# Optimization experiments

Measured on AMD Instinct MI355X. Metric: run time of the kernel, lower is better.

The kernel has to match this reference:

```python
import jax, jax.numpy as jnp
import numpy as np

KS = 63      # Gaussian kernel size (module default)
SIGMA = 32.0 # Gaussian sigma (module default)


def _gaussian_kernel2d(k, sigma):
    # kornia get_gaussian_kernel2d: outer product of normalized 1D gaussians
    x = jnp.arange(k, dtype=jnp.float32) - k // 2
    g = jnp.exp(-(x * x) / (2.0 * sigma * sigma))
    g = g / g.sum()
    return jnp.outer(g, g)  # [k,k]


def _filter2d_constant(x, k2d):
    # kornia filter2d, border_type='constant' (zero pad), depthwise per channel
    C = x.shape[1]
    kern = jnp.broadcast_to(k2d, (C, 1) + k2d.shape)  # [C,1,k,k]
    return jax.lax.conv_general_dilated(
        x, kern, window_strides=(1, 1), padding='SAME',
        dimension_numbers=('NCHW', 'OIHW', 'NCHW'), feature_group_count=C)


def _grid_sample_bilinear(img, grid, align_corners=False):
    # torch.nn.functional.grid_sample, mode='bilinear', padding_mode='zeros'
    B, C, H, W = img.shape
    gx, gy = grid[..., 0], grid[..., 1]
    if align_corners:
        x = (gx + 1.0) * (W - 1) * 0.5
        y = (gy + 1.0) * (H - 1) * 0.5
    else:
        x = ((gx + 1.0) * W - 1.0) * 0.5
        y = ((gy + 1.0) * H - 1.0) * 0.5
    x0 = jnp.floor(x); y0 = jnp.floor(y)
    x0i = x0.astype(jnp.int32); y0i = y0.astype(jnp.int32)
    x1i = x0i + 1; y1i = y0i + 1
    wx1 = x - x0; wx0 = 1.0 - wx1
    wy1 = y - y0; wy0 = 1.0 - wy1

    def gather(iy, ix):
        valid = ((ix >= 0) & (ix < W) & (iy >= 0) & (iy < H))
        iyc = jnp.clip(iy, 0, H - 1)
        ixc = jnp.clip(ix, 0, W - 1)
        # per-batch fancy gather: [B,C,H,W]
        v = jax.vmap(lambda im, yy, xx: im[:, yy, xx])(img, iyc, ixc)
        return v * valid[:, None].astype(img.dtype)

    out = (gather(y0i, x0i) * (wy0 * wx0)[:, None]
           + gather(y0i, x1i) * (wy0 * wx1)[:, None]
           + gather(y1i, x0i) * (wy1 * wx0)[:, None]
           + gather(y1i, x1i) * (wy1 * wx1)[:, None])
    return out


def setup_inputs() -> dict:
    key = jax.random.key(0)
    k1, k2 = jax.random.split(key)
    image = jax.random.normal(k1, (8, 3, 512, 512), dtype=jnp.float32)
    noise = jax.random.uniform(k2, (8, 2, 512, 512), dtype=jnp.float32)
    return {"image": image, "noise": noise}


def reference(image, noise):
    B, C, H, W = image.shape
    noise = noise * 2.0 - 1.0                      # rand*2-1 as in forward()
    k2d = _gaussian_kernel2d(KS, SIGMA)
    disp_xy = _filter2d_constant(noise, k2d)       # [B,2,H,W]
    disp = jnp.transpose(disp_xy, (0, 2, 3, 1))    # [B,H,W,2] (x,y)
    # kornia create_meshgrid(normalized_coordinates=True): linspace(-1,1)
    xs = jnp.linspace(-1.0, 1.0, W, dtype=image.dtype)
    ys = jnp.linspace(-1.0, 1.0, H, dtype=image.dtype)
    base = jnp.stack(jnp.meshgrid(xs, ys, indexing='xy'), axis=-1)  # [H,W,2]
    grid = jnp.clip(base[None] + disp, -1.0, 1.0)
    warped = _grid_sample_bilinear(image, grid, align_corners=False)
    return warped, disp
```

## Files before the change

### kernel.cpp

```cpp
#include <hip/hip_runtime.h>
#include <math.h>

#define KS 63
#define RAD 31
#define NB 8
#define NC 3
#define NH 512
#define NW 512
#define PADH 576
#define TILE_H 32
#define TILE_W 32
#define ROWS 94

struct GaussW { float w[KS]; };

__global__ __launch_bounds__(256) void hblur_kernel(const float* __restrict__ noise,
                                                    float* __restrict__ tmp, GaussW gw) {
    const int bid = blockIdx.x;
    const int t = threadIdx.x;
    if (bid >= NB * NH) {
        const int pid = bid - NB * NH;
        const int img = pid >> 5;
        const int pr  = pid & 31;
        const int row = (pr < 16) ? (pr * 2) : (544 + (pr - 16) * 2);
        float4* dst = (float4*)(tmp + ((size_t)img * PADH + row) * NW);
        dst[t] = make_float4(0.f, 0.f, 0.f, 0.f);
        return;
    }
    const int b = bid >> 9;
    const int h = bid & (NH - 1);
    const int ch = t >> 7;
    const int tt = t & 127;

    __shared__ float rows[2][PADH];
    const float* src = noise + ((size_t)(b * 2 + ch) * NH + h) * NW;
    {
        const float4 nv = *(const float4*)(src + 4 * tt);
        float4 sv;
        sv.x = fmaf(nv.x, 2.f, -1.f); sv.y = fmaf(nv.y, 2.f, -1.f);
        sv.z = fmaf(nv.z, 2.f, -1.f); sv.w = fmaf(nv.w, 2.f, -1.f);
        *(float4*)&rows[ch][32 + 4 * tt] = sv;
        if (tt < 8) {
            *(float4*)&rows[ch][4 * tt]       = make_float4(0.f, 0.f, 0.f, 0.f);
            *(float4*)&rows[ch][544 + 4 * tt] = make_float4(0.f, 0.f, 0.f, 0.f);
        }
    }
    __syncthreads();

    float acc[4] = {0.f, 0.f, 0.f, 0.f};
#pragma unroll
    for (int c = 0; c < 17; ++c) {
        const float4 v = *(const float4*)&rows[ch][4 * tt + 4 * c];
        const float vv[4] = {v.x, v.y, v.z, v.w};
#pragma unroll
        for (int e = 0; e < 4; ++e) {
#pragma unroll
            for (int oo = 0; oo < 4; ++oo) {
                const int j = 4 * c + e - oo - 1;
                if (j >= 0 && j < KS) acc[oo] = fmaf(vv[e], gw.w[j], acc[oo]);
            }
        }
    }
    float4* dst = (float4*)(tmp + (((size_t)(b * 2 + ch) * PADH) + 32 + h) * NW + 4 * tt);
    *dst = make_float4(acc[0], acc[1], acc[2], acc[3]);
}

__global__ __launch_bounds__(256) void vwarp_kernel(const float* __restrict__ tmp,
                                                    const float* __restrict__ img,
                                                    float2* __restrict__ disp,
                                                    float* __restrict__ warped,
                                                    GaussW gw) {
    const int t = threadIdx.x;
    int bid = blockIdx.x;
    bid = (bid & 7) * 256 + (bid >> 3);
    const int b   = bid >> 8;
    const int rem = bid & 255;
    const int ht  = rem >> 4;
    const int wt  = rem & 15;
    const int H0 = ht * TILE_H;
    const int W0 = wt * TILE_W;

    __shared__ float lds[2][ROWS][TILE_W];

    const float* g0 = tmp + ((size_t)(b * 2) * PADH + H0 + 1) * NW + W0;
    const size_t choff = (size_t)PADH * NW;
    for (int idx = t; idx < 2 * ROWS * (TILE_W / 4); idx += 256) {
        const int c4   = idx & 7;
        const int rowc = idx >> 3;
        const int c = (rowc >= ROWS) ? 1 : 0;
        const int r = rowc - ROWS * c;
        const float4 v = *(const float4*)(g0 + (size_t)c * choff + (size_t)r * NW + c4 * 4);
        *(float4*)&lds[c][r][c4 * 4] = v;
    }
    __syncthreads();

    const int w  = t & 31;
    const int lh = (t >> 5) * 4;

    float ax[4] = {0.f, 0.f, 0.f, 0.f};
    float ay[4] = {0.f, 0.f, 0.f, 0.f};
#pragma unroll
    for (int rr = 0; rr < 66; ++rr) {
        const float vx = lds[0][lh + rr][w];
        const float vy = lds[1][lh + rr][w];
#pragma unroll
        for (int o = 0; o < 4; ++o) {
            const int j = rr - o;
            if (j >= 0 && j < KS) {
                ax[o] = fmaf(vx, gw.w[j], ax[o]);
                ay[o] = fmaf(vy, gw.w[j], ay[o]);
            }
        }
    }

    const int wg = W0 + w;
    const float gxb = fmaf((float)wg, 2.0f / 511.0f, -1.0f);
    const float* i0 = img + (size_t)b * NC * NH * NW;
    const float* i1 = i0 + NH * NW;
    const float* i2 = i1 + NH * NW;
    float* wp = warped + (size_t)b * NC * NH * NW;

#pragma unroll
    for (int o = 0; o < 4; ++o) {
        const int h = H0 + lh + o;
        disp[((size_t)b * NH + h) * NW + wg] = make_float2(ax[o], ay[o]);

        float gx = gxb + ax[o];
        float gy = fmaf((float)h, 2.0f / 511.0f, -1.0f) + ay[o];
        gx = fminf(1.f, fmaxf(-1.f, gx));
        gy = fminf(1.f, fmaxf(-1.f, gy));

        const float x = ((gx + 1.0f) * (float)NW - 1.0f) * 0.5f;
        const float y = ((gy + 1.0f) * (float)NH - 1.0f) * 0.5f;
        const float xf = floorf(x), yf = floorf(y);
        const int x0 = (int)xf, y0 = (int)yf;
        const int x1 = x0 + 1,  y1 = y0 + 1;
        const float wx1 = x - xf, wx0 = 1.0f - wx1;
        const float wy1 = y - yf, wy0 = 1.0f - wy1;
        const float fx0 = ((unsigned)x0 < NW) ? 1.f : 0.f;
        const float fx1 = ((unsigned)x1 < NW) ? 1.f : 0.f;
        const float fy0 = ((unsigned)y0 < NH) ? 1.f : 0.f;
        const float fy1 = ((unsigned)y1 < NH) ? 1.f : 0.f;
        const int x0c = min(max(x0, 0), NW - 1), x1c = min(max(x1, 0), NW - 1);
        const int y0c = min(max(y0, 0), NH - 1), y1c = min(max(y1, 0), NH - 1);
        const float w00 = wy0 * wx0 * (fy0 * fx0), w01 = wy0 * wx1 * (fy0 * fx1);
        const float w10 = wy1 * wx0 * (fy1 * fx0), w11 = wy1 * wx1 * (fy1 * fx1);
        const int o00 = y0c * NW + x0c, o01 = y0c * NW + x1c;
        const int o10 = y1c * NW + x0c, o11 = y1c * NW + x1c;
        const size_t po = (size_t)h * NW + wg;
        wp[po]               = ((i0[o00] * w00 + i0[o01] * w01) + i0[o10] * w10) + i0[o11] * w11;
        wp[NH * NW + po]     = ((i1[o00] * w00 + i1[o01] * w01) + i1[o10] * w10) + i1[o11] * w11;
        wp[2 * NH * NW + po] = ((i2[o00] * w00 + i2[o01] * w01) + i2[o10] * w10) + i2[o11] * w11;
    }
}

extern "C" void kernel_launch(void* const* d_in, const int* in_sizes, int n_in,
                              void* d_out, int out_size, void* d_ws, size_t ws_size,
                              hipStream_t stream) {
    const float* image = (const float*)d_in[0];
    const float* noise = (const float*)d_in[1];
    float* warped = (float*)d_out;
    float* dispo  = (float*)d_out + (size_t)NB * NC * NH * NW;
    float* scratch = (float*)d_ws;

    GaussW gw;
    float s = 0.f;
    for (int i = 0; i < KS; ++i) {
        const float xv = (float)(i - RAD);
        gw.w[i] = expf(-(xv * xv) / (2.0f * 32.0f * 32.0f));
        s += gw.w[i];
    }
    for (int i = 0; i < KS; ++i) gw.w[i] /= s;

    hblur_kernel<<<NB * NH + 512, 256, 0, stream>>>(noise, scratch, gw);
    vwarp_kernel<<<NB * (NH / TILE_H) * (NW / TILE_W), 256, 0, stream>>>(
        scratch, image, (float2*)dispo, warped, gw);
}
```

Measured before the change: 136.5 us.

## Widen vertical-warp tiles to 64 columns with 4-wide vectorized per-thread work

The vertical blur and warp kernel now uses 32x64 tiles. Each thread computes 2 rows by 4 adjacent columns, reading float4 values from LDS and writing disp and warped outputs with float4 stores. This cuts LDS reads and store instructions per output and shares each LDS value across fewer redundant loads. The horizontal blur kernel also interleaves batches in its block-to-row mapping. In exchange, LDS use per block doubles and fewer blocks are launched, which can lower occupancy, and the 4-pixel gathers per thread are more serialized.

```diff
diff --git a/kernel.cpp b/kernel.cpp
--- a/kernel.cpp
+++ b/kernel.cpp
@@ -9,7 +9,7 @@
 #define NW 512
 #define PADH 576
 #define TILE_H 32
-#define TILE_W 32
+#define TILE_W 64
 #define ROWS 94
 
 struct GaussW { float w[KS]; };
@@ -27,8 +27,8 @@
         dst[t] = make_float4(0.f, 0.f, 0.f, 0.f);
         return;
     }
-    const int b = bid >> 9;
-    const int h = bid & (NH - 1);
+    const int b = bid & 7;
+    const int h = (bid >> 3) & (NH - 1);
     const int ch = t >> 7;
     const int tt = t & 127;
 
@@ -72,11 +72,11 @@
                                                     GaussW gw) {
     const int t = threadIdx.x;
     int bid = blockIdx.x;
-    bid = (bid & 7) * 256 + (bid >> 3);
-    const int b   = bid >> 8;
-    const int rem = bid & 255;
-    const int ht  = rem >> 4;
-    const int wt  = rem & 15;
+    bid = (bid & 7) * 128 + (bid >> 3);
+    const int b   = bid >> 7;
+    const int rem = bid & 127;
+    const int ht  = rem >> 3;
+    const int wt  = rem & 7;
     const int H0 = ht * TILE_H;
     const int W0 = wt * TILE_W;
 
@@ -85,8 +85,8 @@
     const float* g0 = tmp + ((size_t)(b * 2) * PADH + H0 + 1) * NW + W0;
     const size_t choff = (size_t)PADH * NW;
     for (int idx = t; idx < 2 * ROWS * (TILE_W / 4); idx += 256) {
-        const int c4   = idx & 7;
-        const int rowc = idx >> 3;
+        const int c4   = idx & 15;
+        const int rowc = idx >> 4;
         const int c = (rowc >= ROWS) ? 1 : 0;
         const int r = rowc - ROWS * c;
         const float4 v = *(const float4*)(g0 + (size_t)c * choff + (size_t)r * NW + c4 * 4);
@@ -94,63 +94,82 @@
     }
     __syncthreads();
 
-    const int w  = t & 31;
-    const int lh = (t >> 5) * 4;
+    const int cg = t & 15;
+    const int lh = (t >> 4) * 2;
+    const int w4 = cg * 4;
 
-    float ax[4] = {0.f, 0.f, 0.f, 0.f};
-    float ay[4] = {0.f, 0.f, 0.f, 0.f};
+    float4 ax[2], ay[2];
 #pragma unroll
-    for (int rr = 0; rr < 66; ++rr) {
-        const float vx = lds[0][lh + rr][w];
-        const float vy = lds[1][lh + rr][w];
+    for (int o = 0; o < 2; ++o) {
+        ax[o] = make_float4(0.f, 0.f, 0.f, 0.f);
+        ay[o] = make_float4(0.f, 0.f, 0.f, 0.f);
+    }
 #pragma unroll
-        for (int o = 0; o < 4; ++o) {
+    for (int rr = 0; rr < 64; ++rr) {
+        const float4 vx = *(const float4*)&lds[0][lh + rr][w4];
+        const float4 vy = *(const float4*)&lds[1][lh + rr][w4];
+#pragma unroll
+        for (int o = 0; o < 2; ++o) {
             const int j = rr - o;
             if (j >= 0 && j < KS) {
-                ax[o] = fmaf(vx, gw.w[j], ax[o]);
-                ay[o] = fmaf(vy, gw.w[j], ay[o]);
+                const float wj = gw.w[j];
+                ax[o].x = fmaf(vx.x, wj, ax[o].x); ax[o].y = fmaf(vx.y, wj, ax[o].y);
+                ax[o].z = fmaf(vx.z, wj, ax[o].z); ax[o].w = fmaf(vx.w, wj, ax[o].w);
+                ay[o].x = fmaf(vy.x, wj, ay[o].x); ay[o].y = fmaf(vy.y, wj, ay[o].y);
+                ay[o].z = fmaf(vy.z, wj, ay[o].z); ay[o].w = fmaf(vy.w, wj, ay[o].w);
             }
         }
     }
 
-    const int wg = W0 + w;
-    const float gxb = fmaf((float)wg, 2.0f / 511.0f, -1.0f);
+    const int wg = W0 + w4;
     const float* i0 = img + (size_t)b * NC * NH * NW;
     const float* i1 = i0 + NH * NW;
     const float* i2 = i1 + NH * NW;
     float* wp = warped + (size_t)b * NC * NH * NW;
 
 #pragma unroll
-    for (int o = 0; o < 4; ++o) {
+    for (int o = 0; o < 2; ++o) {
         const int h = H0 + lh + o;
-        disp[((size_t)b * NH + h) * NW + wg] = make_float2(ax[o], ay[o]);
+        float2* drow = disp + ((size_t)b * NH + h) * NW + wg;
+        *(float4*)(drow)     = make_float4(ax[o].x, ay[o].x, ax[o].y, ay[o].y);
+        *(float4*)(drow + 2) = make_float4(ax[o].z, ay[o].z, ax[o].w, ay[o].w);
 
-        float gx = gxb + ax[o];
-        float gy = fmaf((float)h, 2.0f / 511.0f, -1.0f) + ay[o];
-        gx = fminf(1.f, fmaxf(-1.f, gx));
-        gy = fminf(1.f, fmaxf(-1.f, gy));
+        const float gyb = fmaf((float)h, 2.0f / 511.0f, -1.0f);
+        const float axk[4] = {ax[o].x, ax[o].y, ax[o].z, ax[o].w};
+        const float ayk[4] = {ay[o].x, ay[o].y, ay[o].z, ay[o].w};
+        float r0[4], r1[4], r2[4];
+#pragma unroll
+        for (int k = 0; k < 4; ++k) {
+            float gx = fmaf((float)(wg + k), 2.0f / 511.0f, -1.0f) + axk[k];
+            float gy = gyb + ayk[k];
+            gx = fminf(1.f, fmaxf(-1.f, gx));
+            gy = fminf(1.f, fmaxf(-1.f, gy));
 
-        const float x = ((gx + 1.0f) * (float)NW - 1.0f) * 0.5f;
-        const float y = ((gy + 1.0f) * (float)NH - 1.0f) * 0.5f;
-        const float xf = floorf(x), yf = floorf(y);
-        const int x0 = (int)xf, y0 = (int)yf;
-        const int x1 = x0 + 1,  y1 = y0 + 1;
-        const float wx1 = x - xf, wx0 = 1.0f - wx1;
-        const float wy1 = y - yf, wy0 = 1.0f - wy1;
-        const float fx0 = ((unsigned)x0 < NW) ? 1.f : 0.f;
-        const float fx1 = ((unsigned)x1 < NW) ? 1.f : 0.f;
-        const float fy0 = ((unsigned)y0 < NH) ? 1.f : 0.f;
-        const float fy1 = ((unsigned)y1 < NH) ? 1.f : 0.f;
-        const int x0c = min(max(x0, 0), NW - 1), x1c = min(max(x1, 0), NW - 1);
-        const int y0c = min(max(y0, 0), NH - 1), y1c = min(max(y1, 0), NH - 1);
-        const float w00 = wy0 * wx0 * (fy0 * fx0), w01 = wy0 * wx1 * (fy0 * fx1);
-        const float w10 = wy1 * wx0 * (fy1 * fx0), w11 = wy1 * wx1 * (fy1 * fx1);
-        const int o00 = y0c * NW + x0c, o01 = y0c * NW + x1c;
-        const int o10 = y1c * NW + x0c, o11 = y1c * NW + x1c;
+            const float x = ((gx + 1.0f) * (float)NW - 1.0f) * 0.5f;
+            const float y = ((gy + 1.0f) * (float)NH - 1.0f) * 0.5f;
+            const float xf = floorf(x), yf = floorf(y);
+            const int x0 = (int)xf, y0 = (int)yf;
+            const int x1 = x0 + 1,  y1 = y0 + 1;
+            const float wx1 = x - xf, wx0 = 1.0f - wx1;
+            const float wy1 = y - yf, wy0 = 1.0f - wy1;
+            const float fx0 = ((unsigned)x0 < NW) ? 1.f : 0.f;
+            const float fx1 = ((unsigned)x1 < NW) ? 1.f : 0.f;
+            const float fy0 = ((unsigned)y0 < NH) ? 1.f : 0.f;
+            const float fy1 = ((unsigned)y1 < NH) ? 1.f : 0.f;
+            const int x0c = min(max(x0, 0), NW - 1), x1c = min(max(x1, 0), NW - 1);
+            const int y0c = min(max(y0, 0), NH - 1), y1c = min(max(y1, 0), NH - 1);
+            const float w00 = wy0 * wx0 * (fy0 * fx0), w01 = wy0 * wx1 * (fy0 * fx1);
+            const float w10 = wy1 * wx0 * (fy1 * fx0), w11 = wy1 * wx1 * (fy1 * fx1);
+            const int o00 = y0c * NW + x0c, o01 = y0c * NW + x1c;
+            const int o10 = y1c * NW + x0c, o11 = y1c * NW + x1c;
+            r0[k] = ((i0[o00] * w00 + i0[o01] * w01) + i0[o10] * w10) + i0[o11] * w11;
+            r1[k] = ((i1[o00] * w00 + i1[o01] * w01) + i1[o10] * w10) + i1[o11] * w11;
+            r2[k] = ((i2[o00] * w00 + i2[o01] * w01) + i2[o10] * w10) + i2[o11] * w11;
+        }
         const size_t po = (size_t)h * NW + wg;
-        wp[po]               = ((i0[o00] * w00 + i0[o01] * w01) + i0[o10] * w10) + i0[o11] * w11;
-        wp[NH * NW + po]     = ((i1[o00] * w00 + i1[o01] * w01) + i1[o10] * w10) + i1[o11] * w11;
-        wp[2 * NH * NW + po] = ((i2[o00] * w00 + i2[o01] * w01) + i2[o10] * w10) + i2[o11] * w11;
+        *(float4*)(wp + po)               = make_float4(r0[0], r0[1], r0[2], r0[3]);
+        *(float4*)(wp + NH * NW + po)     = make_float4(r1[0], r1[1], r1[2], r1[3]);
+        *(float4*)(wp + 2 * NH * NW + po) = make_float4(r2[0], r2[1], r2[2], r2[3]);
     }
 }
 
```

Measured after the change: 155.1 us. 13.6% more time.
